# Kernel tuning notes

Measured on AMD Instinct MI355X. Metric: run time of the kernel, lower is better.

## Reference

```python
import jax, jax.numpy as jnp
import numpy as np

N = 100_000      # nodes
E = 1_600_000    # edges (avg degree 16)
F_IN = 128       # in_feats
H = 128          # n_hidden
H2 = 64          # n_hidden // 2


def setup_inputs() -> dict:
    key = jax.random.key(0)
    k1, k2, k3, k4, k5 = jax.random.split(key, 5)
    features = jax.random.normal(k1, (N, F_IN), dtype=jnp.float32)
    W1 = jax.random.normal(k2, (F_IN, H), dtype=jnp.float32) * 0.05
    W2 = jax.random.normal(k3, (H, H2), dtype=jnp.float32) * 0.05
    src = jax.random.randint(k4, (E,), 0, N, dtype=jnp.int32)
    dst = jax.random.randint(k5, (E,), 0, N, dtype=jnp.int32)
    return {"features": features, "W1": W1, "W2": W2, "src": src, "dst": dst}


def _graph_conv(h, W, src, dst, out_norm, in_norm):
    # DGL GraphConv, norm='both', bias=False:
    #   rst = D_dst^{-1/2} * (A @ (D_src^{-1/2} * h)) @ W
    # (weight applied before/after aggregation is mathematically identical)
    h = h * out_norm[:, None]                                   # scale source feats
    agg = jax.ops.segment_sum(h[src], dst, num_segments=N)      # SpMM: sum over in-edges
    return (agg * in_norm[:, None]) @ W


def reference(features, W1, W2, src, dst):
    ones = jnp.ones(src.shape[0], dtype=jnp.float32)
    # allow_zero_in_degree=True -> DGL clamps degrees to min 1 for norm
    out_deg = jnp.clip(jax.ops.segment_sum(ones, src, num_segments=N), 1.0)
    in_deg = jnp.clip(jax.ops.segment_sum(ones, dst, num_segments=N), 1.0)
    out_norm = out_deg ** -0.5
    in_norm = in_deg ** -0.5
    h = _graph_conv(features, W1, src, dst, out_norm, in_norm)  # [N, H]
    h = jax.nn.relu(h)
    return _graph_conv(h, W2, src, dst, out_norm, in_norm)      # [N, H2]
```

## Files before the change

kernel.cpp:

```cpp
#include <hip/hip_runtime.h>
#include <cstdint>
#include <cstddef>

#define NN 100000
#define NE 1600000
#define FD 128
#define HD2 64

#define BSH 7
#define BSZ 128
#define NB ((NN + BSZ - 1) / BSZ)
#define TILE 4096
#define NTILE ((NE + TILE - 1) / TILE)
#define CAPB 2560
#define NPREP ((NN * 32 + FD * 64 + HD2 * 64 + 255) / 256)

static_assert(NB <= 1024, "bucket scan assumes <=1024 buckets");

typedef short bf16x8_t __attribute__((ext_vector_type(8)));
typedef float f32x4_t __attribute__((ext_vector_type(4)));
typedef unsigned char uchar;

static __device__ __forceinline__ uint f2bf(float x) {
  uint u = __float_as_uint(x);
  return (u + 0x7fffu + ((u >> 16) & 1u)) >> 16;
}
static __device__ __forceinline__ uint pack2(float lo, float hi) {
  return f2bf(lo) | (f2bf(hi) << 16);
}
static __device__ __forceinline__ float bflo(uint v) { return __uint_as_float(v << 16); }
static __device__ __forceinline__ float bfhi(uint v) { return __uint_as_float(v & 0xffff0000u); }

static __device__ __forceinline__ float dec_w(uint r) {
  return __uint_as_float(((r >> 17) + 0x38000u) << 12);
}

static __device__ __forceinline__ void wave_lds_fence() {
  asm volatile("s_waitcnt lgkmcnt(0)" ::: "memory");
  __builtin_amdgcn_sched_barrier(0);
}

__global__ void k_bucket_prep(const int* __restrict__ src, const int* __restrict__ dst,
                              int* __restrict__ bcnt_d, int* __restrict__ bcnt_s,
                              uint* __restrict__ brec_d, uchar* __restrict__ brec_s,
                              const float* __restrict__ feat, uint* __restrict__ Xraw,
                              const float* __restrict__ W1, const float* __restrict__ W2,
                              uint* __restrict__ W1t, uint* __restrict__ W2t) {
  __shared__ int h[NB];
  __shared__ int gb[NB];
  __shared__ int ls[NB];
  __shared__ int psum[256];
  __shared__ int ntot;
  __shared__ ushort bkt[TILE];
  __shared__ uint lrec[TILE];
  const int bid = blockIdx.x;
  const int t = threadIdx.x;
  if (bid >= 2 * NTILE) {
    int i = (bid - 2 * NTILE) * 256 + t;
    if (i < NN * 32) {
      float4 f = *(const float4*)(feat + 4 * (size_t)i);
      uint2 o;
      o.x = pack2(f.x, f.y);
      o.y = pack2(f.z, f.w);
      *(uint2*)(Xraw + 2 * (size_t)i) = o;
    } else {
      int j = i - NN * 32;
      if (j < FD * 64) {
        int n = j >> 6, kk = j & 63;
        W1t[j] = pack2(W1[(size_t)(2 * kk) * FD + n], W1[(size_t)(2 * kk + 1) * FD + n]);
      } else if (j < FD * 64 + HD2 * 64) {
        int j2 = j - FD * 64;
        int n = j2 >> 6, kk = j2 & 63;
        W2t[j2] = pack2(W2[(size_t)(2 * kk) * HD2 + n], W2[(size_t)(2 * kk + 1) * HD2 + n]);
      }
    }
    return;
  }
  const bool is_dst = bid < NTILE;
  const int* key = is_dst ? dst : src;
  const int base = (is_dst ? bid : bid - NTILE) * TILE;
  for (int i = t; i < NB; i += 256) h[i] = 0;
  __syncthreads();
  for (int i = t; i < TILE; i += 256) {
    int e = base + i;
    if (e < NE) atomicAdd(&h[key[e] >> BSH], 1);
  }
  __syncthreads();
  int* bcnt = is_dst ? bcnt_d : bcnt_s;
  for (int i = t; i < NB; i += 256) {
    int c = h[i];
    gb[i] = c ? atomicAdd(bcnt + i, c) : 0;
  }
  int i0 = t * 4;
  int c0 = (i0 + 0 < NB) ? h[i0 + 0] : 0;
  int c1 = (i0 + 1 < NB) ? h[i0 + 1] : 0;
  int c2 = (i0 + 2 < NB) ? h[i0 + 2] : 0;
  int c3 = (i0 + 3 < NB) ? h[i0 + 3] : 0;
  int cs = c0 + c1 + c2 + c3;
  psum[t] = cs;
  __syncthreads();
#pragma unroll
  for (int off = 1; off < 256; off <<= 1) {
    int x = (t >= off) ? psum[t - off] : 0;
    __syncthreads();
    psum[t] += x;
    __syncthreads();
  }
  int excl = psum[t] - cs;
  if (i0 + 0 < NB) ls[i0 + 0] = excl;
  if (i0 + 1 < NB) ls[i0 + 1] = excl + c0;
  if (i0 + 2 < NB) ls[i0 + 2] = excl + c0 + c1;
  if (i0 + 3 < NB) ls[i0 + 3] = excl + c0 + c1 + c2;
  if (t == 255) ntot = psum[255];
  __syncthreads();
  for (int i = t; i < NB; i += 256) h[i] = 0;
  __syncthreads();
  if (is_dst) {
    for (int i = t; i < TILE; i += 256) {
      int e = base + i;
      if (e < NE) {
        int d = dst[e], sv = src[e];
        int b = d >> BSH;
        int q = ls[b] + atomicAdd(&h[b], 1);
        lrec[q] = ((uint)(d & (BSZ - 1)) << 17) | (uint)sv;
        bkt[q] = (ushort)b;
      }
    }
  } else {
    for (int i = t; i < TILE; i += 256) {
      int e = base + i;
      if (e < NE) {
        int sv = src[e];
        int b = sv >> BSH;
        int q = ls[b] + atomicAdd(&h[b], 1);
        lrec[q] = (uint)(sv & (BSZ - 1));
        bkt[q] = (ushort)b;
      }
    }
  }
  __syncthreads();
  const int n = ntot;
  if (is_dst) {
    for (int q = t; q < n; q += 256) {
      int b = bkt[q];
      int p = gb[b] + (q - ls[b]);
      if (p < CAPB) brec_d[(size_t)b * CAPB + p] = lrec[q];
    }
  } else {
    for (int q = t; q < n; q += 256) {
      int b = bkt[q];
      int p = gb[b] + (q - ls[b]);
      if (p < CAPB) brec_s[(size_t)b * CAPB + p] = (uchar)lrec[q];
    }
  }
}

__global__ __launch_bounds__(1024) void k_onorm_scan(const uchar* __restrict__ brec_s,
                                                     const int* __restrict__ bcnt_s,
                                                     float* __restrict__ out_norm,
                                                     const int* __restrict__ bcnt_d,
                                                     int* __restrict__ boff_d) {
  __shared__ int sm[1024];
  const int t = threadIdx.x;
  const int b = blockIdx.x;
  if (b < NB) {
    if (t < BSZ) sm[t] = 0;
    __syncthreads();
    const int len = min(bcnt_s[b], CAPB);
    const size_t rbase = (size_t)b * CAPB;
    for (int e = t; e < len; e += 1024)
      atomicAdd(&sm[brec_s[rbase + e]], 1);
    __syncthreads();
    const int s0 = b * BSZ;
    const int ns = min(BSZ, NN - s0);
    if (t < ns) out_norm[s0 + t] = rsqrtf((float)max(sm[t], 1));
  } else {
    int v = (t < NB) ? bcnt_d[t] : 0;
    sm[t] = v;
    __syncthreads();
#pragma unroll
    for (int off = 1; off < 1024; off <<= 1) {
      int x = (t >= off) ? sm[t - off] : 0;
      __syncthreads();
      sm[t] += x;
      __syncthreads();
    }
    if (t < NB) boff_d[t + 1] = sm[t];
    if (t == 0) boff_d[0] = 0;
  }
}

__global__ __launch_bounds__(256) void k_build(const uint* __restrict__ brec_d,
                                               const int* __restrict__ bcnt_d,
                                               const int* __restrict__ boff,
                                               const float* __restrict__ onorm,
                                               int* __restrict__ row_ptr,
                                               float* __restrict__ in_norm,
                                               uint* __restrict__ csr) {
  __shared__ int lcnt[BSZ];
  __shared__ int lscan[BSZ + 1];
  __shared__ int lcur[BSZ];
  __shared__ int lcsr[CAPB];
  const int t = threadIdx.x;
  const int b = blockIdx.x;
  const int d0 = b * BSZ;
  const int nd = min(BSZ, NN - d0);
  const size_t rbase = (size_t)b * CAPB;
  const int len = min(bcnt_d[b], CAPB);
  const int ebase = boff[b];

  for (int i = t; i < BSZ; i += 256) lcnt[i] = 0;
  __syncthreads();
  for (int e = t; e < len; e += 256)
    atomicAdd(&lcnt[brec_d[rbase + e] >> 17], 1);
  __syncthreads();
  for (int i = t; i < nd; i += 256)
    in_norm[d0 + i] = rsqrtf((float)max(lcnt[i], 1));

  if (t < BSZ) lcur[t] = lcnt[t];
  __syncthreads();
#pragma unroll
  for (int off = 1; off < BSZ; off <<= 1) {
    int x = (t >= off && t < BSZ) ? lcur[t - off] : 0;
    __syncthreads();
    if (t < BSZ) lcur[t] += x;
    __syncthreads();
  }
  if (t < BSZ) lscan[t + 1] = lcur[t];
  if (t == 0) lscan[0] = 0;
  __syncthreads();
  for (int i = t; i <= nd; i += 256) row_ptr[d0 + i] = ebase + lscan[i];
  if (t < BSZ) lcur[t] = lscan[t];
  __syncthreads();

  for (int e = t; e < len; e += 256) {
    uint r = brec_d[rbase + e];
    int p = atomicAdd(&lcur[r >> 17], 1);
    lcsr[p] = (int)(r & 0x1FFFFu);
  }
  __syncthreads();
  for (int ld = t; ld < nd; ld += 256) {
    int a = lscan[ld], bnd = lscan[ld + 1];
    for (int i = a + 1; i < bnd; ++i) {
      int v = lcsr[i];
      int j = i - 1;
      while (j >= a && lcsr[j] > v) { lcsr[j + 1] = lcsr[j]; --j; }
      lcsr[j + 1] = v;
    }
  }
  __syncthreads();
  for (int i = t; i < len; i += 256) {
    int s = lcsr[i];
    uint code = (__float_as_uint(onorm[s]) >> 12) - 0x38000u;
    csr[ebase + i] = (code << 17) | (uint)s;
  }
}

__global__ __launch_bounds__(256) void k_spmm_mlp(const uint* __restrict__ Xraw,
                                                  const int* __restrict__ row_ptr,
                                                  const uint* __restrict__ csr,
                                                  const float* __restrict__ in_norm,
                                                  const uint* __restrict__ W1t,
                                                  const uint* __restrict__ W2t,
                                                  const float* __restrict__ onorm,
                                                  ushort* __restrict__ Tb) {
  __shared__ ushort h_lds[4 * 16 * FD];
  const int tid = threadIdx.x;
  const int wid = tid >> 6;
  const int lane = tid & 63;
  const int grp = lane >> 4;
  const int gl = lane & 15;
  const int l15 = lane & 15;
  const int g = lane >> 4;
  const int rowbase = blockIdx.x * 64 + wid * 16;
  char* const lds = (char*)h_lds + wid * 4096;

  for (int i = 0; i < 16; ++i) {
    const int row = rowbase + i;
    float2 a0 = {0.f, 0.f}, a1 = {0.f, 0.f}, a2 = {0.f, 0.f}, a3 = {0.f, 0.f};
    if (row < NN) {
      int e0 = row_ptr[row], e1 = row_ptr[row + 1];
#define ACCW(v, ww)                                                       \
  a0.x = fmaf(ww, bflo((v).x), a0.x); a0.y = fmaf(ww, bfhi((v).x), a0.y); \
  a1.x = fmaf(ww, bflo((v).y), a1.x); a1.y = fmaf(ww, bfhi((v).y), a1.y); \
  a2.x = fmaf(ww, bflo((v).z), a2.x); a2.y = fmaf(ww, bfhi((v).z), a2.y); \
  a3.x = fmaf(ww, bflo((v).w), a3.x); a3.y = fmaf(ww, bfhi((v).w), a3.y);
      int e = e0;
      for (; e + 16 <= e1; e += 16) {
        uint r0 = csr[e + grp];
        uint r1 = csr[e + 4 + grp];
        uint r2 = csr[e + 8 + grp];
        uint r3 = csr[e + 12 + grp];
        uint4 v0 = *(const uint4*)(Xraw + ((size_t)(r0 & 0x1FFFFu) << 6) + (gl << 2));
        uint4 v1 = *(const uint4*)(Xraw + ((size_t)(r1 & 0x1FFFFu) << 6) + (gl << 2));
        uint4 v2 = *(const uint4*)(Xraw + ((size_t)(r2 & 0x1FFFFu) << 6) + (gl << 2));
        uint4 v3 = *(const uint4*)(Xraw + ((size_t)(r3 & 0x1FFFFu) << 6) + (gl << 2));
        float w0 = dec_w(r0), w1 = dec_w(r1), w2 = dec_w(r2), w3 = dec_w(r3);
        ACCW(v0, w0);
        ACCW(v1, w1);
        ACCW(v2, w2);
        ACCW(v3, w3);
      }
      for (; e + 4 <= e1; e += 4) {
        uint r0 = csr[e + grp];
        uint4 v0 = *(const uint4*)(Xraw + ((size_t)(r0 & 0x1FFFFu) << 6) + (gl << 2));
        float w0 = dec_w(r0);
        ACCW(v0, w0);
      }
      if (e + grp < e1) {
        uint r0 = csr[e + grp];
        uint4 v0 = *(const uint4*)(Xraw + ((size_t)(r0 & 0x1FFFFu) << 6) + (gl << 2));
        float w0 = dec_w(r0);
        ACCW(v0, w0);
      }
#undef ACCW
#pragma unroll
      for (int m = 16; m <= 32; m <<= 1) {
        a0.x += __shfl_xor(a0.x, m); a0.y += __shfl_xor(a0.y, m);
        a1.x += __shfl_xor(a1.x, m); a1.y += __shfl_xor(a1.y, m);
        a2.x += __shfl_xor(a2.x, m); a2.y += __shfl_xor(a2.y, m);
        a3.x += __shfl_xor(a3.x, m); a3.y += __shfl_xor(a3.y, m);
      }
    }
    if (grp == 0) {
      uint4 o = {0u, 0u, 0u, 0u};
      if (row < NN) {
        float wi = in_norm[row];
        o.x = pack2(a0.x * wi, a0.y * wi);
        o.y = pack2(a1.x * wi, a1.y * wi);
        o.z = pack2(a2.x * wi, a2.y * wi);
        o.w = pack2(a3.x * wi, a3.y * wi);
      }
      int byte = i * 256 + gl * 16;
      byte ^= (i & 7) << 4;
      *(uint4*)(lds + byte) = o;
    }
  }
  wave_lds_fence();

  bf16x8_t afr[4];
#pragma unroll
  for (int kc = 0; kc < 4; ++kc) {
    int byte = l15 * 256 + kc * 64 + g * 16;
    byte ^= (l15 & 7) << 4;
    afr[kc] = *(const bf16x8_t*)(lds + byte);
  }
  float wnorm[4];
#pragma unroll
  for (int r = 0; r < 4; ++r)
    wnorm[r] = onorm[min(rowbase + 4 * g + r, NN - 1)];
  wave_lds_fence();

#pragma unroll
  for (int nf = 0; nf < 8; ++nf) {
    f32x4_t acc = {0.f, 0.f, 0.f, 0.f};
#pragma unroll
    for (int kc = 0; kc < 4; ++kc) {
      bf16x8_t b = *(const bf16x8_t*)(W1t + (size_t)(nf * 16 + l15) * 64 + kc * 16 + g * 4);
      acc = __builtin_amdgcn_mfma_f32_16x16x32_bf16(afr[kc], b, acc, 0, 0, 0);
    }
#pragma unroll
    for (int r = 0; r < 4; ++r) {
      float hv = fmaxf(acc[r], 0.f) * wnorm[r];
      int rl = 4 * g + r;
      int byte = rl * 256 + (nf * 16 + l15) * 2;
      byte ^= (rl & 7) << 4;
      *(ushort*)(lds + byte) = (ushort)f2bf(hv);
    }
  }
  wave_lds_fence();

  bf16x8_t a2f[4];
#pragma unroll
  for (int kc = 0; kc < 4; ++kc) {
    int byte = l15 * 256 + (kc * 32 + 8 * g) * 2;
    byte ^= (l15 & 7) << 4;
    a2f[kc] = *(const bf16x8_t*)(lds + byte);
  }
#pragma unroll
  for (int nf = 0; nf < 4; ++nf) {
    f32x4_t acc = {0.f, 0.f, 0.f, 0.f};
#pragma unroll
    for (int kc = 0; kc < 4; ++kc) {
      bf16x8_t b = *(const bf16x8_t*)(W2t + (size_t)(nf * 16 + l15) * 64 + kc * 16 + g * 4);
      acc = __builtin_amdgcn_mfma_f32_16x16x32_bf16(a2f[kc], b, acc, 0, 0, 0);
    }
#pragma unroll
    for (int r = 0; r < 4; ++r) {
      int row = rowbase + 4 * g + r;
      if (row < NN)
        Tb[(size_t)row * HD2 + nf * 16 + l15] = (ushort)f2bf(acc[r]);
    }
  }
}

__global__ void k_spmm2b(const uint* __restrict__ Tb, const int* __restrict__ row_ptr,
                         const uint* __restrict__ csr, const float* __restrict__ in_norm,
                         float* __restrict__ out) {
  int gid = blockIdx.x * blockDim.x + threadIdx.x;
  int row = gid >> 6;
  if (row >= NN) return;
  int lane = threadIdx.x & 63;
  int grp = lane >> 4;
  int gl = lane & 15;
  int e0 = row_ptr[row], e1 = row_ptr[row + 1];
  float2 a0 = {0.f, 0.f}, a1 = {0.f, 0.f};
#define ACC2(v)                                  \
  a0.x += bflo((v).x); a0.y += bfhi((v).x);      \
  a1.x += bflo((v).y); a1.y += bfhi((v).y);
  int e = e0;
  for (; e + 16 <= e1; e += 16) {
    uint s0 = csr[e + grp] & 0x1FFFFu;
    uint s1 = csr[e + 4 + grp] & 0x1FFFFu;
    uint s2 = csr[e + 8 + grp] & 0x1FFFFu;
    uint s3 = csr[e + 12 + grp] & 0x1FFFFu;
    uint2 v0 = *(const uint2*)(Tb + ((size_t)s0 << 5) + (gl << 1));
    uint2 v1 = *(const uint2*)(Tb + ((size_t)s1 << 5) + (gl << 1));
    uint2 v2 = *(const uint2*)(Tb + ((size_t)s2 << 5) + (gl << 1));
    uint2 v3 = *(const uint2*)(Tb + ((size_t)s3 << 5) + (gl << 1));
    ACC2(v0);
    ACC2(v1);
    ACC2(v2);
    ACC2(v3);
  }
  for (; e + 4 <= e1; e += 4) {
    uint s0 = csr[e + grp] & 0x1FFFFu;
    uint2 v0 = *(const uint2*)(Tb + ((size_t)s0 << 5) + (gl << 1));
    ACC2(v0);
  }
  if (e + grp < e1) {
    uint s0 = csr[e + grp] & 0x1FFFFu;
    uint2 v0 = *(const uint2*)(Tb + ((size_t)s0 << 5) + (gl << 1));
    ACC2(v0);
  }
#undef ACC2
#pragma unroll
  for (int m = 16; m <= 32; m <<= 1) {
    a0.x += __shfl_xor(a0.x, m); a0.y += __shfl_xor(a0.y, m);
    a1.x += __shfl_xor(a1.x, m); a1.y += __shfl_xor(a1.y, m);
  }
  if (grp == 0) {
    float wi = in_norm[row];
    *(float4*)(out + (size_t)row * HD2 + gl * 4) =
        make_float4(a0.x * wi, a0.y * wi, a1.x * wi, a1.y * wi);
  }
}

extern "C" void kernel_launch(void* const* d_in, const int* in_sizes, int n_in,
                              void* d_out, int out_size, void* d_ws, size_t ws_size,
                              hipStream_t stream) {
  const float* feat = (const float*)d_in[0];
  const float* W1   = (const float*)d_in[1];
  const float* W2   = (const float*)d_in[2];
  const int*   src  = (const int*)d_in[3];
  const int*   dst  = (const int*)d_in[4];
  float* out = (float*)d_out;

  char* p = (char*)d_ws;
  auto take = [&p](size_t bytes) -> char* {
    char* r = p;
    p += (bytes + 511) & ~(size_t)511;
    return r;
  };
  int*   row_ptr  = (int*)take((size_t)(NN + 1) * 4);
  int*   bcnt     = (int*)take((size_t)2 * NB * 4);
  int*   boff_d   = (int*)take((size_t)(NB + 1) * 4);
  float* out_norm = (float*)take((size_t)NN * 4);
  float* in_norm  = (float*)take((size_t)NN * 4);
  uint*  csr      = (uint*)take((size_t)NE * 4);
  uint*  W1t      = (uint*)take((size_t)FD * 64 * 4);
  uint*  W2t      = (uint*)take((size_t)HD2 * 64 * 4);
  uint*  Xraw     = (uint*)take((size_t)NN * 64 * 4);
  uint*  recbuf   = (uint*)take((size_t)NB * CAPB * 4 + (size_t)NB * CAPB);
  ushort* Tb      = (ushort*)take((size_t)NN * HD2 * 2);
  int*   bcnt_d   = bcnt;
  int*   bcnt_s   = bcnt + NB;
  uint*   brec_d  = recbuf;
  uchar*  brec_s  = (uchar*)(recbuf + (size_t)NB * CAPB);

  hipMemsetAsync(bcnt, 0, (size_t)2 * NB * 4, stream);

  k_bucket_prep<<<2 * NTILE + NPREP, 256, 0, stream>>>(src, dst, bcnt_d, bcnt_s, brec_d, brec_s,
                                                       feat, Xraw, W1, W2, W1t, W2t);
  k_onorm_scan <<<NB + 1, 1024, 0, stream>>>(brec_s, bcnt_s, out_norm, bcnt_d, boff_d);
  k_build      <<<NB, 256, 0, stream>>>(brec_d, bcnt_d, boff_d, out_norm,
                                        row_ptr, in_norm, csr);

  k_spmm_mlp<<<(NN + 63) / 64, 256, 0, stream>>>(Xraw, row_ptr, csr, in_norm,
                                                 W1t, W2t, out_norm, Tb);
  k_spmm2b  <<<(NN * 64) / 256, 256, 0, stream>>>((const uint*)Tb, row_ptr, csr,
                                                  in_norm, out);
}
```

Baseline: 276.2 us.

## Assign one row per 16-lane group in SpMM instead of splitting edges

```diff
diff --git a/kernel.cpp b/kernel.cpp
--- a/kernel.cpp
+++ b/kernel.cpp
@@ -268,73 +268,67 @@
   const int tid = threadIdx.x;
   const int wid = tid >> 6;
   const int lane = tid & 63;
-  const int grp = lane >> 4;
   const int gl = lane & 15;
   const int l15 = lane & 15;
   const int g = lane >> 4;
   const int rowbase = blockIdx.x * 64 + wid * 16;
   char* const lds = (char*)h_lds + wid * 4096;
 
-  for (int i = 0; i < 16; ++i) {
-    const int row = rowbase + i;
+  for (int i = 0; i < 4; ++i) {
+    const int rl = i * 4 + g;
+    const int row = rowbase + rl;
     float2 a0 = {0.f, 0.f}, a1 = {0.f, 0.f}, a2 = {0.f, 0.f}, a3 = {0.f, 0.f};
+    int e0 = 0, e1 = 0;
     if (row < NN) {
-      int e0 = row_ptr[row], e1 = row_ptr[row + 1];
+      e0 = row_ptr[row];
+      e1 = row_ptr[row + 1];
+    }
 #define ACCW(v, ww)                                                       \
   a0.x = fmaf(ww, bflo((v).x), a0.x); a0.y = fmaf(ww, bfhi((v).x), a0.y); \
   a1.x = fmaf(ww, bflo((v).y), a1.x); a1.y = fmaf(ww, bfhi((v).y), a1.y); \
   a2.x = fmaf(ww, bflo((v).z), a2.x); a2.y = fmaf(ww, bfhi((v).z), a2.y); \
   a3.x = fmaf(ww, bflo((v).w), a3.x); a3.y = fmaf(ww, bfhi((v).w), a3.y);
-      int e = e0;
-      for (; e + 16 <= e1; e += 16) {
-        uint r0 = csr[e + grp];
-        uint r1 = csr[e + 4 + grp];
-        uint r2 = csr[e + 8 + grp];
-        uint r3 = csr[e + 12 + grp];
-        uint4 v0 = *(const uint4*)(Xraw + ((size_t)(r0 & 0x1FFFFu) << 6) + (gl << 2));
-        uint4 v1 = *(const uint4*)(Xraw + ((size_t)(r1 & 0x1FFFFu) << 6) + (gl << 2));
-        uint4 v2 = *(const uint4*)(Xraw + ((size_t)(r2 & 0x1FFFFu) << 6) + (gl << 2));
-        uint4 v3 = *(const uint4*)(Xraw + ((size_t)(r3 & 0x1FFFFu) << 6) + (gl << 2));
-        float w0 = dec_w(r0), w1 = dec_w(r1), w2 = dec_w(r2), w3 = dec_w(r3);
-        ACCW(v0, w0);
-        ACCW(v1, w1);
-        ACCW(v2, w2);
-        ACCW(v3, w3);
-      }
-      for (; e + 4 <= e1; e += 4) {
-        uint r0 = csr[e + grp];
-        uint4 v0 = *(const uint4*)(Xraw + ((size_t)(r0 & 0x1FFFFu) << 6) + (gl << 2));
-        float w0 = dec_w(r0);
-        ACCW(v0, w0);
-      }
-      if (e + grp < e1) {
-        uint r0 = csr[e + grp];
-        uint4 v0 = *(const uint4*)(Xraw + ((size_t)(r0 & 0x1FFFFu) << 6) + (gl << 2));
-        float w0 = dec_w(r0);
-        ACCW(v0, w0);
-      }
+    int e = e0;
+    for (; e + 8 <= e1; e += 8) {
+      uint r0 = csr[e + 0], r1 = csr[e + 1], r2 = csr[e + 2], r3 = csr[e + 3];
+      uint r4 = csr[e + 4], r5 = csr[e + 5], r6 = csr[e + 6], r7 = csr[e + 7];
+      uint4 v0 = *(const uint4*)(Xraw + ((size_t)(r0 & 0x1FFFFu) << 6) + (gl << 2));
+      uint4 v1 = *(const uint4*)(Xraw + ((size_t)(r1 & 0x1FFFFu) << 6) + (gl << 2));
+      uint4 v2 = *(const uint4*)(Xraw + ((size_t)(r2 & 0x1FFFFu) << 6) + (gl << 2));
+      uint4 v3 = *(const uint4*)(Xraw + ((size_t)(r3 & 0x1FFFFu) << 6) + (gl << 2));
+      uint4 v4 = *(const uint4*)(Xraw + ((size_t)(r4 & 0x1FFFFu) << 6) + (gl << 2));
+      uint4 v5 = *(const uint4*)(Xraw + ((size_t)(r5 & 0x1FFFFu) << 6) + (gl << 2));
+      uint4 v6 = *(const uint4*)(Xraw + ((size_t)(r6 & 0x1FFFFu) << 6) + (gl << 2));
+      uint4 v7 = *(const uint4*)(Xraw + ((size_t)(r7 & 0x1FFFFu) << 6) + (gl << 2));
+      float w0 = dec_w(r0), w1 = dec_w(r1), w2 = dec_w(r2), w3 = dec_w(r3);
+      float w4 = dec_w(r4), w5 = dec_w(r5), w6 = dec_w(r6), w7 = dec_w(r7);
+      ACCW(v0, w0);
+      ACCW(v1, w1);
+      ACCW(v2, w2);
+      ACCW(v3, w3);
+      ACCW(v4, w4);
+      ACCW(v5, w5);
+      ACCW(v6, w6);
+      ACCW(v7, w7);
+    }
+    for (; e < e1; ++e) {
+      uint r0 = csr[e];
+      uint4 v0 = *(const uint4*)(Xraw + ((size_t)(r0 & 0x1FFFFu) << 6) + (gl << 2));
+      float w0 = dec_w(r0);
+      ACCW(v0, w0);
+    }
 #undef ACCW
-#pragma unroll
-      for (int m = 16; m <= 32; m <<= 1) {
-        a0.x += __shfl_xor(a0.x, m); a0.y += __shfl_xor(a0.y, m);
-        a1.x += __shfl_xor(a1.x, m); a1.y += __shfl_xor(a1.y, m);
-        a2.x += __shfl_xor(a2.x, m); a2.y += __shfl_xor(a2.y, m);
-        a3.x += __shfl_xor(a3.x, m); a3.y += __shfl_xor(a3.y, m);
-      }
-    }
-    if (grp == 0) {
-      uint4 o = {0u, 0u, 0u, 0u};
-      if (row < NN) {
-        float wi = in_norm[row];
-        o.x = pack2(a0.x * wi, a0.y * wi);
-        o.y = pack2(a1.x * wi, a1.y * wi);
-        o.z = pack2(a2.x * wi, a2.y * wi);
-        o.w = pack2(a3.x * wi, a3.y * wi);
-      }
-      int byte = i * 256 + gl * 16;
-      byte ^= (i & 7) << 4;
-      *(uint4*)(lds + byte) = o;
-    }
+    uint4 o = {0u, 0u, 0u, 0u};
+    if (row < NN) {
+      float wi = in_norm[row];
+      o.x = pack2(a0.x * wi, a0.y * wi);
+      o.y = pack2(a1.x * wi, a1.y * wi);
+      o.z = pack2(a2.x * wi, a2.y * wi);
+      o.w = pack2(a3.x * wi, a3.y * wi);
+    }
+    int byte = rl * 256 + gl * 16;
+    byte ^= (rl & 7) << 4;
+    *(uint4*)(lds + byte) = o;
   }
   wave_lds_fence();
 
```

Measured after the change: 250.8 us. 9.2% less time.
